# Optimization experiments

Hardware: AMD Instinct MI355X
Metric: run time of the kernel (lower is better)

The kernel has to match this reference:

```python
import jax, jax.numpy as jnp
import numpy as np
import math

D = 768
H = 8
DK = D // H
FF = 1024
EPS = 1e-5


def _layer_norm(x, g, b):
    m = jnp.mean(x, axis=-1, keepdims=True)
    v = jnp.mean((x - m) ** 2, axis=-1, keepdims=True)
    return (x - m) * jax.lax.rsqrt(v + EPS) * g + b


def _mha(x, attention_mask, Wq, bq, Wv, bv, g, b):
    # x: (B,S,D); attention_mask: (B,S,1) bool (True = masked/padding query row)
    B, S, _ = x.shape
    q = (x @ Wq + bq).reshape(B, S, H, DK).transpose(0, 2, 1, 3)  # (B,H,S,dk)
    # NOTE: original code uses the V projection for BOTH k and v (k = self.V(x))
    kv = (x @ Wv + bv).reshape(B, S, H, DK).transpose(0, 2, 1, 3)
    k = kv
    v = kv
    w = jnp.einsum('bhqd,bhkd->bhqk', q, k) / math.sqrt(DK)  # (B,H,S,S)
    pad = attention_mask[:, None, :, :]                      # (B,1,S,1) -> bcast (B,1,S,S)
    causal = jnp.triu(jnp.ones((S, S), dtype=bool), k=1)     # look-ahead mask
    mask = pad | causal
    w = jnp.where(mask, jnp.float32(-1e9), w)
    # NOTE: original uses nn.Softmax(dim=2) -> softmax over the QUERY axis
    score = jax.nn.softmax(w, axis=2)
    o = jnp.einsum('bhqk,bhkd->bhqd', score, v)              # (B,H,S,dk)
    o = o.transpose(0, 2, 1, 3).reshape(B, S, D)
    return _layer_norm(o + x, g, b)


def _ffn(x, W1, b1, W2, b2, g, b):
    h = jax.nn.relu(x @ W1 + b1)
    return _layer_norm(h @ W2 + b2 + x, g, b)


def setup_inputs() -> dict:
    key = jax.random.key(0)
    ks = jax.random.split(key, 16)
    B, S = 8, 1024
    sc = 0.02
    inp = {
        'x': jax.random.normal(ks[0], (B, S, D), dtype=jnp.float32),
        'attention_mask': jax.random.randint(ks[1], (B, S, 1), 0, 2).astype(bool),
    }
    for i, pre in enumerate(['a1', 'a2']):
        inp[pre + '_Wq'] = jax.random.normal(ks[2 + 4 * i], (D, D), dtype=jnp.float32) * sc
        inp[pre + '_bq'] = jnp.zeros((D,), dtype=jnp.float32)
        inp[pre + '_Wv'] = jax.random.normal(ks[3 + 4 * i], (D, D), dtype=jnp.float32) * sc
        inp[pre + '_bv'] = jnp.zeros((D,), dtype=jnp.float32)
        inp[pre + '_g'] = jnp.ones((D,), dtype=jnp.float32)
        inp[pre + '_b'] = jnp.zeros((D,), dtype=jnp.float32)
    inp['f_W1'] = jax.random.normal(ks[10], (D, FF), dtype=jnp.float32) * sc
    inp['f_b1'] = jnp.zeros((FF,), dtype=jnp.float32)
    inp['f_W2'] = jax.random.normal(ks[11], (FF, D), dtype=jnp.float32) * sc
    inp['f_b2'] = jnp.zeros((D,), dtype=jnp.float32)
    inp['f_g'] = jnp.ones((D,), dtype=jnp.float32)
    inp['f_b'] = jnp.zeros((D,), dtype=jnp.float32)
    return inp


def reference(x, attention_mask,
              a1_Wq, a1_bq, a1_Wv, a1_bv, a1_g, a1_b,
              a2_Wq, a2_bq, a2_Wv, a2_bv, a2_g, a2_b,
              f_W1, f_b1, f_W2, f_b2, f_g, f_b):
    x = _mha(x, attention_mask, a1_Wq, a1_bq, a1_Wv, a1_bv, a1_g, a1_b)
    x = _mha(x, attention_mask, a2_Wq, a2_bq, a2_Wv, a2_bv, a2_g, a2_b)
    x = _ffn(x, f_W1, f_b1, f_W2, f_b2, f_g, f_b)
    return x
```

## Files before the change

### kernel.cpp

```cpp
#include <hip/hip_runtime.h>
#include <cstddef>

#define BB 8
#define SS 1024
#define DD 768
#define HH 8
#define DKK 96
#define FFF 1024
#define MM (BB*SS)
#define QVW 1536
#define SM_SCALE 0.10206207261596577f
#define NTILES 16
#define NPAIR  136

typedef unsigned short ushort_t;
typedef short short8 __attribute__((ext_vector_type(8)));
typedef float f32x4 __attribute__((ext_vector_type(4)));
typedef ushort_t us4 __attribute__((ext_vector_type(4)));

__device__ __forceinline__ ushort_t f2b(float f) {
    union { float f; unsigned u; } x; x.f = f;
    unsigned r = x.u + 0x7fffu + ((x.u >> 16) & 1u);
    return (ushort_t)(r >> 16);
}
__device__ __forceinline__ float b2f(ushort_t u) {
    union { unsigned u; float f; } x; x.u = ((unsigned)u) << 16;
    return x.f;
}
__device__ __forceinline__ void gload16(const ushort_t* g, void* lds_base) {
    __builtin_amdgcn_global_load_lds(
        (const __attribute__((address_space(1))) unsigned int*)g,
        (__attribute__((address_space(3))) unsigned int*)lds_base, 16, 0, 0);
}

__global__ __launch_bounds__(256) void castWT(
    const float* __restrict__ W, ushort_t* __restrict__ Wt, int K, int N)
{
    __shared__ float T[32][33];
    const int tx = threadIdx.x & 31, ty = threadIdx.x >> 5;
    const int n0 = blockIdx.x * 32, k0 = blockIdx.y * 32;
    #pragma unroll
    for (int r = 0; r < 4; ++r)
        T[ty + 8*r][tx] = W[(size_t)(k0 + ty + 8*r) * N + n0 + tx];
    __syncthreads();
    #pragma unroll
    for (int r = 0; r < 4; ++r)
        Wt[(size_t)(n0 + ty + 8*r) * K + k0 + tx] = f2b(T[tx][ty + 8*r]);
}

__global__ __launch_bounds__(256) void castWT4(
    const float* __restrict__ Wa, const float* __restrict__ Wb,
    const float* __restrict__ Wc, const float* __restrict__ Wd,
    ushort_t* __restrict__ Ta, ushort_t* __restrict__ Tb,
    ushort_t* __restrict__ Tc, ushort_t* __restrict__ Td)
{
    __shared__ float T[32][33];
    const float* W; ushort_t* Wt;
    switch (blockIdx.z) {
        case 0:  W = Wa; Wt = Ta; break;
        case 1:  W = Wb; Wt = Tb; break;
        case 2:  W = Wc; Wt = Tc; break;
        default: W = Wd; Wt = Td; break;
    }
    const int tx = threadIdx.x & 31, ty = threadIdx.x >> 5;
    const int n0 = blockIdx.x * 32, k0 = blockIdx.y * 32;
    #pragma unroll
    for (int r = 0; r < 4; ++r)
        T[ty + 8*r][tx] = W[(size_t)(k0 + ty + 8*r) * DD + n0 + tx];
    __syncthreads();
    #pragma unroll
    for (int r = 0; r < 4; ++r)
        Wt[(size_t)(n0 + ty + 8*r) * DD + k0 + tx] = f2b(T[tx][ty + 8*r]);
}

__global__ __launch_bounds__(256) void cast_f2b(
    const float* __restrict__ in, ushort_t* __restrict__ out, int n4)
{
    const int i = blockIdx.x * 256 + threadIdx.x;
    if (i >= n4) return;
    const float4 v = ((const float4*)in)[i];
    us4 o; o.x = f2b(v.x); o.y = f2b(v.y); o.z = f2b(v.z); o.w = f2b(v.w);
    ((us4*)out)[i] = o;
}

template<int RELU>
__global__ __launch_bounds__(256) void gemm_bt(
    const ushort_t* __restrict__ A, const ushort_t* __restrict__ Bt,
    const float* __restrict__ bias, const float* __restrict__ bias2, int bN,
    ushort_t* __restrict__ C, int K, int N)
{
    __shared__ ushort_t S[128*136];
    ushort_t* As = S;
    ushort_t* Bs = S + 128*64;
    const int tid  = threadIdx.x;
    const int lane = tid & 63, wave = tid >> 6;
    const int wm = wave >> 1, wn = wave & 1;
    const int n = lane & 15, quad = lane >> 4;
    const int sx = n & 7;
    const int bm = blockIdx.y * 128, bn = blockIdx.x * 128;

    f32x4 acc[4][4];
    #pragma unroll
    for (int i = 0; i < 4; ++i)
        #pragma unroll
        for (int j = 0; j < 4; ++j) acc[i][j] = (f32x4){0.f, 0.f, 0.f, 0.f};

    for (int k0 = 0; k0 < K; k0 += 64) {
        #pragma unroll
        for (int it = 0; it < 4; ++it) {
            const int u   = (it*4 + wave)*64 + lane;
            const int row = u >> 3;
            const int c   = (u & 7) ^ (row & 7);
            gload16(A  + (size_t)(bm + row) * K + k0 + c*8, (char*)As + (it*4 + wave)*1024);
            gload16(Bt + (size_t)(bn + row) * K + k0 + c*8, (char*)Bs + (it*4 + wave)*1024);
        }
        __syncthreads();
        #pragma unroll
        for (int ks = 0; ks < 2; ++ks) {
            short8 af[4], bf[4];
            #pragma unroll
            for (int i = 0; i < 4; ++i)
                af[i] = *(short8*)&As[((wm*64 + i*16 + n)*8 + ((ks*4 + quad) ^ sx))*8];
            #pragma unroll
            for (int j = 0; j < 4; ++j)
                bf[j] = *(short8*)&Bs[((wn*64 + j*16 + n)*8 + ((ks*4 + quad) ^ sx))*8];
            #pragma unroll
            for (int i = 0; i < 4; ++i)
                #pragma unroll
                for (int j = 0; j < 4; ++j)
                    acc[i][j] = __builtin_amdgcn_mfma_f32_16x16x32_bf16(af[i], bf[j], acc[i][j], 0, 0, 0);
        }
        __syncthreads();
    }
    #pragma unroll
    for (int j = 0; j < 4; ++j) {
        const int col = wn*64 + j*16 + n;
        const int gcol = bn + col;
        const float bsv = (gcol < bN) ? bias[gcol] : bias2[gcol - bN];
        #pragma unroll
        for (int i = 0; i < 4; ++i) {
            const int lrow = wm*64 + i*16 + quad*4;
            #pragma unroll
            for (int r = 0; r < 4; ++r) {
                float v = acc[i][j][r] + bsv;
                if (RELU) v = fmaxf(v, 0.f);
                S[(lrow + r)*136 + col] = f2b(v);
            }
        }
    }
    __syncthreads();
    #pragma unroll
    for (int it = 0; it < 8; ++it) {
        const int u = it*256 + tid;
        const int grow = u >> 4, gc = u & 15;
        *(short8*)(C + (size_t)(bm + grow)*N + bn + gc*8) = *(short8*)&S[grow*136 + gc*8];
    }
}

__global__ __launch_bounds__(256) void attn_scores(
    const ushort_t* __restrict__ QV, const int* __restrict__ amask,
    ushort_t* __restrict__ E, float* __restrict__ lpart)
{
    __shared__ ushort_t Qs[64*128];
    __shared__ ushort_t Ks[64*128];
    __shared__ ushort_t Etile[64*72];
    __shared__ float colsum[4][64];
    __shared__ float padf[64];
    const int tid = threadIdx.x, lane = tid & 63, wave = tid >> 6;
    const int n = lane & 15, quad = lane >> 4;
    const int sx = n & 7;
    const int t = blockIdx.x;
    int qt = (int)((-1.f + sqrtf(1.f + 8.f*(float)t)) * 0.5f);
    if ((qt+1)*(qt+2)/2 <= t) ++qt;
    if (qt*(qt+1)/2 > t) --qt;
    const int kt = t - qt*(qt+1)/2;
    const int q0 = qt*64, k0 = kt*64;
    const int h = blockIdx.y, b = blockIdx.z;
    const ushort_t* Qh = QV + (size_t)b*SS*QVW + h*DKK;
    const ushort_t* Kh = QV + (size_t)b*SS*QVW + DD + h*DKK;

    #pragma unroll
    for (int it = 0; it < 4; ++it) {
        const int u = (it*4 + wave)*64 + lane;
        const int row = u >> 4;
        const int c = (u & 15) ^ (row & 7);
        if (c < 12) {
            gload16(Qh + (size_t)(q0 + row)*QVW + c*8, (char*)Qs + (it*4 + wave)*1024);
            gload16(Kh + (size_t)(k0 + row)*QVW + c*8, (char*)Ks + (it*4 + wave)*1024);
        }
    }
    if (tid < 64) padf[tid] = (amask[b*SS + q0 + tid] != 0) ? 1.f : 0.f;
    __syncthreads();

    ushort_t* Et = E + (size_t)(b*HH + h)*NPAIR*4096 + (size_t)(qt*(qt+1)/2 + kt)*4096;

    #pragma unroll
    for (int ns = 0; ns < 4; ++ns) {
        f32x4 sa = (f32x4){0.f, 0.f, 0.f, 0.f};
        #pragma unroll
        for (int ks = 0; ks < 3; ++ks) {
            const short8 aq = *(short8*)&Qs[((wave*16 + n)*16 + ((ks*4 + quad) ^ sx))*8];
            const short8 bk = *(short8*)&Ks[((ns*16   + n)*16 + ((ks*4 + quad) ^ sx))*8];
            sa = __builtin_amdgcn_mfma_f32_16x16x32_bf16(aq, bk, sa, 0, 0, 0);
        }
        const int kl = ns*16 + n;
        const int keyg = k0 + kl;
        float s = 0.f;
        #pragma unroll
        for (int r = 0; r < 4; ++r) {
            const int qrow = wave*16 + quad*4 + r;
            const bool dead = (padf[qrow] != 0.f) || (keyg > q0 + qrow);
            const float e = dead ? 0.f : __expf(sa[r] * SM_SCALE);
            s += e;
            Etile[qrow*72 + kl] = f2b(e);
        }
        s += __shfl_xor(s, 16);
        s += __shfl_xor(s, 32);
        if (quad == 0) colsum[wave][kl] = s;
    }
    __syncthreads();
    #pragma unroll
    for (int it = 0; it < 2; ++it) {
        const int u = it*256 + tid;
        const int grow = u >> 3, gc = u & 7;
        *(short8*)(Et + grow*64 + gc*8) = *(short8*)&Etile[grow*72 + gc*8];
    }
    if (tid < 64) {
        const float s = colsum[0][tid] + colsum[1][tid] + colsum[2][tid] + colsum[3][tid];
        lpart[((size_t)(b*HH + h)*NTILES + qt)*SS + k0 + tid] = s;
    }
}

__global__ __launch_bounds__(256) void transpose_scale(
    const ushort_t* __restrict__ QV, const float* __restrict__ lpart,
    ushort_t* __restrict__ Vt)
{
    __shared__ ushort_t T[64][104];
    __shared__ float rlv[64];
    const int tid = threadIdx.x;
    const int k0 = blockIdx.x * 64, h = blockIdx.y, b = blockIdx.z;
    const ushort_t* src = QV + (size_t)b*SS*QVW + DD + h*DKK;
    for (int s = tid; s < 768; s += 256) {
        const int r = s / 12, c = s % 12;
        *(short8*)&T[r][c*8] = *(const short8*)(src + (size_t)(k0 + r)*QVW + c*8);
    }
    if (tid < 64) {
        const float* lp = lpart + (size_t)(b*HH + h)*NTILES*SS;
        float l = 0.f;
        for (int qt = k0 >> 6; qt < NTILES; ++qt) l += lp[(size_t)qt*SS + k0 + tid];
        rlv[tid] = (l > 0.f) ? (1.f / l) : 0.f;
    }
    __syncthreads();
    ushort_t* dst = Vt + ((size_t)b*HH + h)*DKK*SS;
    for (int s = tid; s < 768; s += 256) {
        const int dk = s >> 3, c = s & 7;
        short8 v;
        #pragma unroll
        for (int i = 0; i < 8; ++i)
            v[i] = (short)f2b(b2f(T[c*8 + i][dk]) * rlv[c*8 + i]);
        *(short8*)(dst + (size_t)dk*SS + k0 + c*8) = v;
    }
}

__global__ __launch_bounds__(256) void attn_pv(
    const ushort_t* __restrict__ E, const ushort_t* __restrict__ Vt,
    ushort_t* __restrict__ O)
{
    __shared__ ushort_t Es[64*64];
    __shared__ ushort_t Vs[96*64];
    const int tid = threadIdx.x, lane = tid & 63, wave = tid >> 6;
    const int n = lane & 15, quad = lane >> 4;
    const int sx = n & 7;
    const int px = blockIdx.x;
    const int h = blockIdx.y, b = blockIdx.z;
    const ushort_t* Eb  = E + (size_t)(b*HH + h)*NPAIR*4096;
    const ushort_t* Vth = Vt + ((size_t)b*HH + h)*DKK*SS;

    #pragma unroll
    for (int half = 0; half < 2; ++half) {
        const int qt = half ? (15 - px) : px;
        const int q0 = qt * 64;
        f32x4 acc[6];
        #pragma unroll
        for (int t = 0; t < 6; ++t) acc[t] = (f32x4){0.f, 0.f, 0.f, 0.f};
        const ushort_t* Eq = Eb + (size_t)(qt*(qt+1)/2)*4096;

        for (int kt = 0; kt <= qt; ++kt) {
            const ushort_t* Et = Eq + (size_t)kt*4096;
            #pragma unroll
            for (int it = 0; it < 2; ++it) {
                const int u = (it*4 + wave)*64 + lane;
                const int row = u >> 3, c = (u & 7) ^ (row & 7);
                gload16(Et + (size_t)row*64 + c*8, (char*)Es + (it*4 + wave)*1024);
            }
            #pragma unroll
            for (int it = 0; it < 3; ++it) {
                const int u = (it*4 + wave)*64 + lane;
                const int row = u >> 3, c = (u & 7) ^ (row & 7);
                gload16(Vth + (size_t)row*SS + kt*64 + c*8, (char*)Vs + (it*4 + wave)*1024);
            }
            __syncthreads();
            #pragma unroll
            for (int kk = 0; kk < 2; ++kk) {
                const short8 ae = *(short8*)&Es[((wave*16 + n)*8 + ((kk*4 + quad) ^ sx))*8];
                #pragma unroll
                for (int nt = 0; nt < 6; ++nt) {
                    const short8 bv = *(short8*)&Vs[((nt*16 + n)*8 + ((kk*4 + quad) ^ sx))*8];
                    acc[nt] = __builtin_amdgcn_mfma_f32_16x16x32_bf16(ae, bv, acc[nt], 0, 0, 0);
                }
            }
            __syncthreads();
        }
        #pragma unroll
        for (int nt = 0; nt < 6; ++nt) {
            #pragma unroll
            for (int r = 0; r < 4; ++r) {
                const int q = q0 + wave*16 + quad*4 + r;
                O[((size_t)b*SS + q)*DD + h*DKK + nt*16 + n] = f2b(acc[nt][r]);
            }
        }
    }
}

__device__ __forceinline__ float block_sum256(float s, float* tmp4)
{
    #pragma unroll
    for (int off = 32; off > 0; off >>= 1) s += __shfl_down(s, off);
    __syncthreads();
    if ((threadIdx.x & 63) == 0) tmp4[threadIdx.x >> 6] = s;
    __syncthreads();
    return tmp4[0] + tmp4[1] + tmp4[2] + tmp4[3];
}

template<int XBF, int RBF, int OUTF32>
__global__ __launch_bounds__(256) void resid_ln(
    const void* __restrict__ X, const void* __restrict__ R,
    const float* __restrict__ g, const float* __restrict__ beta,
    ushort_t* __restrict__ OutB, float* __restrict__ OutF)
{
    __shared__ float tmp4[4];
    const int row = blockIdx.x;
    const int tid = threadIdx.x;
    float v[3], s = 0.f;
    #pragma unroll
    for (int i = 0; i < 3; ++i) {
        const size_t idx = (size_t)row * DD + tid + 256*i;
        const float xv = XBF ? b2f(((const ushort_t*)X)[idx]) : ((const float*)X)[idx];
        const float rv = RBF ? b2f(((const ushort_t*)R)[idx]) : ((const float*)R)[idx];
        v[i] = xv + rv;
        s += v[i];
    }
    const float mu = block_sum256(s, tmp4) * (1.f / DD);
    float qv = 0.f;
    #pragma unroll
    for (int i = 0; i < 3; ++i) { const float d = v[i] - mu; qv += d * d; }
    const float inv = rsqrtf(block_sum256(qv, tmp4) * (1.f / DD) + 1e-5f);
    #pragma unroll
    for (int i = 0; i < 3; ++i) {
        const int c = tid + 256*i;
        const float o = (v[i] - mu) * inv * g[c] + beta[c];
        if (OUTF32) OutF[(size_t)row * DD + c] = o;
        else        OutB[(size_t)row * DD + c] = f2b(o);
    }
}

extern "C" void kernel_launch(void* const* d_in, const int* in_sizes, int n_in,
                              void* d_out, int out_size, void* d_ws, size_t ws_size,
                              hipStream_t stream)
{
    (void)in_sizes; (void)n_in; (void)out_size; (void)ws_size;
    const float* x0    = (const float*)d_in[0];
    const int*   amask = (const int*)d_in[1];
    const float* a1_Wq = (const float*)d_in[2];
    const float* a1_bq = (const float*)d_in[3];
    const float* a1_Wv = (const float*)d_in[4];
    const float* a1_bv = (const float*)d_in[5];
    const float* a1_g  = (const float*)d_in[6];
    const float* a1_b  = (const float*)d_in[7];
    const float* a2_Wq = (const float*)d_in[8];
    const float* a2_bq = (const float*)d_in[9];
    const float* a2_Wv = (const float*)d_in[10];
    const float* a2_bv = (const float*)d_in[11];
    const float* a2_g  = (const float*)d_in[12];
    const float* a2_b  = (const float*)d_in[13];
    const float* f_W1  = (const float*)d_in[14];
    const float* f_b1  = (const float*)d_in[15];
    const float* f_W2  = (const float*)d_in[16];
    const float* f_b2  = (const float*)d_in[17];
    const float* f_g   = (const float*)d_in[18];
    const float* f_b   = (const float*)d_in[19];

    char* ws = (char*)d_ws;
    size_t off = 0;
    auto alloc = [&](size_t bytes) { void* p = ws + off; off += (bytes + 255) & ~(size_t)255; return p; };
    ushort_t* WqvT1 = (ushort_t*)alloc((size_t)QVW*DD*2);
    ushort_t* WqvT2 = (ushort_t*)alloc((size_t)QVW*DD*2);
    ushort_t* W1T   = (ushort_t*)alloc((size_t)DD*FFF*2);
    ushort_t* W2T   = (ushort_t*)alloc((size_t)DD*FFF*2);
    ushort_t* xb0   = (ushort_t*)alloc((size_t)MM*DD*2);
    ushort_t* xb1   = (ushort_t*)alloc((size_t)MM*DD*2);
    ushort_t* xb2   = (ushort_t*)alloc((size_t)MM*DD*2);
    ushort_t* Ob    = (ushort_t*)alloc((size_t)MM*DD*2);
    ushort_t* QVb   = (ushort_t*)alloc((size_t)MM*QVW*2);
    ushort_t* hb    = QVb;
    ushort_t* Vtb   = (ushort_t*)alloc((size_t)MM*DD*2);
    float* lpart = (float*)alloc((size_t)BB*HH*NTILES*SS*4);
    ushort_t* Ebuf = (ushort_t*)alloc((size_t)BB*HH*NPAIR*4096*2);
    float* out = (float*)d_out;

    const dim3 blk(256);
    const dim3 gsc(NPAIR, HH, BB);
    const dim3 gpv(NTILES/2, HH, BB);
    const dim3 gtr(SS/64, HH, BB);
    const dim3 gqv(QVW/128, MM/128);
    const dim3 gf1(FFF/128, MM/128);
    const dim3 gf2(DD/128, MM/128);

    castWT4<<<dim3(DD/32, DD/32, 4), blk, 0, stream>>>(
        a1_Wq, a1_Wv, a2_Wq, a2_Wv,
        WqvT1, WqvT1 + (size_t)DD*DD, WqvT2, WqvT2 + (size_t)DD*DD);
    castWT<<<dim3(FFF/32, DD/32), blk, 0, stream>>>(f_W1, W1T, DD, FFF);
    castWT<<<dim3(DD/32, FFF/32), blk, 0, stream>>>(f_W2, W2T, FFF, DD);
    cast_f2b<<<(MM*DD/4 + 255)/256, blk, 0, stream>>>(x0, xb0, MM*DD/4);

    gemm_bt<0><<<gqv, blk, 0, stream>>>(xb0, WqvT1, a1_bq, a1_bv, DD, QVb, DD, QVW);
    attn_scores<<<gsc, blk, 0, stream>>>(QVb, amask, Ebuf, lpart);
    transpose_scale<<<gtr, blk, 0, stream>>>(QVb, lpart, Vtb);
    attn_pv<<<gpv, blk, 0, stream>>>(Ebuf, Vtb, Ob);
    resid_ln<1,0,0><<<dim3(MM), blk, 0, stream>>>(Ob, x0, a1_g, a1_b, xb1, nullptr);

    gemm_bt<0><<<gqv, blk, 0, stream>>>(xb1, WqvT2, a2_bq, a2_bv, DD, QVb, DD, QVW);
    attn_scores<<<gsc, blk, 0, stream>>>(QVb, amask, Ebuf, lpart);
    transpose_scale<<<gtr, blk, 0, stream>>>(QVb, lpart, Vtb);
    attn_pv<<<gpv, blk, 0, stream>>>(Ebuf, Vtb, Ob);
    resid_ln<1,1,0><<<dim3(MM), blk, 0, stream>>>(Ob, xb1, a2_g, a2_b, xb2, nullptr);

    gemm_bt<1><<<gf1, blk, 0, stream>>>(xb2, W1T, f_b1, f_b1, FFF, hb, DD, FFF);
    gemm_bt<0><<<gf2, blk, 0, stream>>>(hb, W2T, f_b2, f_b2, DD, Ob, FFF, DD);
    resid_ln<1,1,1><<<dim3(MM), blk, 0, stream>>>(Ob, xb2, f_g, f_b, nullptr, out);
}
```

Baseline: 407.1 us.

## Split attention PV over key ranges, load Q/K directly to registers, merge weight casts

attn_pv now splits each query tile's key loop into two halves handled by separate blocks. Each half writes its own partial output buffer, and resid_ln sums the two partials, which doubles the grid to improve occupancy. attn_scores drops its LDS staging of Q/K and reads MFMA fragments straight from global memory with per-lane mask loads. The three weight-cast launches are merged into one. The costs are extra partial-output traffic, idle early-exit blocks in the cast kernel, and uncoalesced fragment loads in attn_scores.

```diff
diff --git a/kernel.cpp b/kernel.cpp
--- a/kernel.cpp
+++ b/kernel.cpp
@@ -33,12 +33,27 @@
         (__attribute__((address_space(3))) unsigned int*)lds_base, 16, 0, 0);
 }
 
-__global__ __launch_bounds__(256) void castWT(
-    const float* __restrict__ W, ushort_t* __restrict__ Wt, int K, int N)
+__global__ __launch_bounds__(256) void castW_all(
+    const float* __restrict__ Wq1, const float* __restrict__ Wv1,
+    const float* __restrict__ Wq2, const float* __restrict__ Wv2,
+    const float* __restrict__ W1,  const float* __restrict__ W2,
+    ushort_t* __restrict__ Tq1, ushort_t* __restrict__ Tv1,
+    ushort_t* __restrict__ Tq2, ushort_t* __restrict__ Tv2,
+    ushort_t* __restrict__ T1,  ushort_t* __restrict__ T2)
 {
     __shared__ float T[32][33];
+    const float* W; ushort_t* Wt; int K, N;
+    switch (blockIdx.z) {
+        case 0:  W = Wq1; Wt = Tq1; K = DD;  N = DD;  break;
+        case 1:  W = Wv1; Wt = Tv1; K = DD;  N = DD;  break;
+        case 2:  W = Wq2; Wt = Tq2; K = DD;  N = DD;  break;
+        case 3:  W = Wv2; Wt = Tv2; K = DD;  N = DD;  break;
+        case 4:  W = W1;  Wt = T1;  K = DD;  N = FFF; break;
+        default: W = W2;  Wt = T2;  K = FFF; N = DD;  break;
+    }
+    const int n0 = blockIdx.x * 32, k0 = blockIdx.y * 32;
+    if (n0 >= N || k0 >= K) return;
     const int tx = threadIdx.x & 31, ty = threadIdx.x >> 5;
-    const int n0 = blockIdx.x * 32, k0 = blockIdx.y * 32;
     #pragma unroll
     for (int r = 0; r < 4; ++r)
         T[ty + 8*r][tx] = W[(size_t)(k0 + ty + 8*r) * N + n0 + tx];
@@ -46,31 +61,6 @@
     #pragma unroll
     for (int r = 0; r < 4; ++r)
         Wt[(size_t)(n0 + ty + 8*r) * K + k0 + tx] = f2b(T[tx][ty + 8*r]);
-}
-
-__global__ __launch_bounds__(256) void castWT4(
-    const float* __restrict__ Wa, const float* __restrict__ Wb,
-    const float* __restrict__ Wc, const float* __restrict__ Wd,
-    ushort_t* __restrict__ Ta, ushort_t* __restrict__ Tb,
-    ushort_t* __restrict__ Tc, ushort_t* __restrict__ Td)
-{
-    __shared__ float T[32][33];
-    const float* W; ushort_t* Wt;
-    switch (blockIdx.z) {
-        case 0:  W = Wa; Wt = Ta; break;
-        case 1:  W = Wb; Wt = Tb; break;
-        case 2:  W = Wc; Wt = Tc; break;
-        default: W = Wd; Wt = Td; break;
-    }
-    const int tx = threadIdx.x & 31, ty = threadIdx.x >> 5;
-    const int n0 = blockIdx.x * 32, k0 = blockIdx.y * 32;
-    #pragma unroll
-    for (int r = 0; r < 4; ++r)
-        T[ty + 8*r][tx] = W[(size_t)(k0 + ty + 8*r) * DD + n0 + tx];
-    __syncthreads();
-    #pragma unroll
-    for (int r = 0; r < 4; ++r)
-        Wt[(size_t)(n0 + ty + 8*r) * DD + k0 + tx] = f2b(T[tx][ty + 8*r]);
 }
 
 __global__ __launch_bounds__(256) void cast_f2b(
@@ -161,14 +151,10 @@
     const ushort_t* __restrict__ QV, const int* __restrict__ amask,
     ushort_t* __restrict__ E, float* __restrict__ lpart)
 {
-    __shared__ ushort_t Qs[64*128];
-    __shared__ ushort_t Ks[64*128];
     __shared__ ushort_t Etile[64*72];
     __shared__ float colsum[4][64];
-    __shared__ float padf[64];
     const int tid = threadIdx.x, lane = tid & 63, wave = tid >> 6;
     const int n = lane & 15, quad = lane >> 4;
-    const int sx = n & 7;
     const int t = blockIdx.x;
     int qt = (int)((-1.f + sqrtf(1.f + 8.f*(float)t)) * 0.5f);
     if ((qt+1)*(qt+2)/2 <= t) ++qt;
@@ -179,37 +165,30 @@
     const ushort_t* Qh = QV + (size_t)b*SS*QVW + h*DKK;
     const ushort_t* Kh = QV + (size_t)b*SS*QVW + DD + h*DKK;
 
-    #pragma unroll
-    for (int it = 0; it < 4; ++it) {
-        const int u = (it*4 + wave)*64 + lane;
-        const int row = u >> 4;
-        const int c = (u & 15) ^ (row & 7);
-        if (c < 12) {
-            gload16(Qh + (size_t)(q0 + row)*QVW + c*8, (char*)Qs + (it*4 + wave)*1024);
-            gload16(Kh + (size_t)(k0 + row)*QVW + c*8, (char*)Ks + (it*4 + wave)*1024);
-        }
-    }
-    if (tid < 64) padf[tid] = (amask[b*SS + q0 + tid] != 0) ? 1.f : 0.f;
-    __syncthreads();
-
-    ushort_t* Et = E + (size_t)(b*HH + h)*NPAIR*4096 + (size_t)(qt*(qt+1)/2 + kt)*4096;
+    const ushort_t* Qrow = Qh + (size_t)(q0 + wave*16 + n)*QVW + quad*8;
+    const short8 qf0 = *(const short8*)(Qrow);
+    const short8 qf1 = *(const short8*)(Qrow + 32);
+    const short8 qf2 = *(const short8*)(Qrow + 64);
+
+    int deadq[4];
+    #pragma unroll
+    for (int r = 0; r < 4; ++r)
+        deadq[r] = amask[b*SS + q0 + wave*16 + quad*4 + r];
 
     #pragma unroll
     for (int ns = 0; ns < 4; ++ns) {
+        const ushort_t* Krow = Kh + (size_t)(k0 + ns*16 + n)*QVW + quad*8;
         f32x4 sa = (f32x4){0.f, 0.f, 0.f, 0.f};
-        #pragma unroll
-        for (int ks = 0; ks < 3; ++ks) {
-            const short8 aq = *(short8*)&Qs[((wave*16 + n)*16 + ((ks*4 + quad) ^ sx))*8];
-            const short8 bk = *(short8*)&Ks[((ns*16   + n)*16 + ((ks*4 + quad) ^ sx))*8];
-            sa = __builtin_amdgcn_mfma_f32_16x16x32_bf16(aq, bk, sa, 0, 0, 0);
-        }
+        sa = __builtin_amdgcn_mfma_f32_16x16x32_bf16(qf0, *(const short8*)(Krow),      sa, 0, 0, 0);
+        sa = __builtin_amdgcn_mfma_f32_16x16x32_bf16(qf1, *(const short8*)(Krow + 32), sa, 0, 0, 0);
+        sa = __builtin_amdgcn_mfma_f32_16x16x32_bf16(qf2, *(const short8*)(Krow + 64), sa, 0, 0, 0);
         const int kl = ns*16 + n;
         const int keyg = k0 + kl;
         float s = 0.f;
         #pragma unroll
         for (int r = 0; r < 4; ++r) {
             const int qrow = wave*16 + quad*4 + r;
-            const bool dead = (padf[qrow] != 0.f) || (keyg > q0 + qrow);
+            const bool dead = (deadq[r] != 0) || (keyg > q0 + qrow);
             const float e = dead ? 0.f : __expf(sa[r] * SM_SCALE);
             s += e;
             Etile[qrow*72 + kl] = f2b(e);
@@ -219,6 +198,8 @@
         if (quad == 0) colsum[wave][kl] = s;
     }
     __syncthreads();
+
+    ushort_t* Et = E + (size_t)(b*HH + h)*NPAIR*4096 + (size_t)(qt*(qt+1)/2 + kt)*4096;
     #pragma unroll
     for (int it = 0; it < 2; ++it) {
         const int u = it*256 + tid;
@@ -264,15 +245,16 @@
 
 __global__ __launch_bounds__(256) void attn_pv(
     const ushort_t* __restrict__ E, const ushort_t* __restrict__ Vt,
-    ushort_t* __restrict__ O)
+    ushort_t* __restrict__ O0, ushort_t* __restrict__ O1)
 {
     __shared__ ushort_t Es[64*64];
     __shared__ ushort_t Vs[96*64];
     const int tid = threadIdx.x, lane = tid & 63, wave = tid >> 6;
     const int n = lane & 15, quad = lane >> 4;
     const int sx = n & 7;
-    const int px = blockIdx.x;
+    const int px = blockIdx.x >> 1, s = blockIdx.x & 1;
     const int h = blockIdx.y, b = blockIdx.z;
+    ushort_t* O = s ? O1 : O0;
     const ushort_t* Eb  = E + (size_t)(b*HH + h)*NPAIR*4096;
     const ushort_t* Vth = Vt + ((size_t)b*HH + h)*DKK*SS;
 
@@ -280,12 +262,15 @@
     for (int half = 0; half < 2; ++half) {
         const int qt = half ? (15 - px) : px;
         const int q0 = qt * 64;
+        const int m   = (qt + 2) >> 1;
+        const int klo = s ? m : 0;
+        const int khi = s ? qt + 1 : m;
         f32x4 acc[6];
         #pragma unroll
         for (int t = 0; t < 6; ++t) acc[t] = (f32x4){0.f, 0.f, 0.f, 0.f};
         const ushort_t* Eq = Eb + (size_t)(qt*(qt+1)/2)*4096;
 
-        for (int kt = 0; kt <= qt; ++kt) {
+        for (int kt = klo; kt < khi; ++kt) {
             const ushort_t* Et = Eq + (size_t)kt*4096;
             #pragma unroll
             for (int it = 0; it < 2; ++it) {
@@ -332,11 +317,12 @@
     return tmp4[0] + tmp4[1] + tmp4[2] + tmp4[3];
 }
 
-template<int XBF, int RBF, int OUTF32>
+template<int XBF, int RBF, int OUTF32, int HAS2>
 __global__ __launch_bounds__(256) void resid_ln(
     const void* __restrict__ X, const void* __restrict__ R,
     const float* __restrict__ g, const float* __restrict__ beta,
-    ushort_t* __restrict__ OutB, float* __restrict__ OutF)
+    ushort_t* __restrict__ OutB, float* __restrict__ OutF,
+    const ushort_t* __restrict__ X2)
 {
     __shared__ float tmp4[4];
     const int row = blockIdx.x;
@@ -347,7 +333,8 @@
         const size_t idx = (size_t)row * DD + tid + 256*i;
         const float xv = XBF ? b2f(((const ushort_t*)X)[idx]) : ((const float*)X)[idx];
         const float rv = RBF ? b2f(((const ushort_t*)R)[idx]) : ((const float*)R)[idx];
-        v[i] = xv + rv;
+        const float x2 = HAS2 ? b2f(X2[idx]) : 0.f;
+        v[i] = xv + x2 + rv;
         s += v[i];
     }
     const float mu = block_sum256(s, tmp4) * (1.f / DD);
@@ -400,7 +387,8 @@
     ushort_t* xb0   = (ushort_t*)alloc((size_t)MM*DD*2);
     ushort_t* xb1   = (ushort_t*)alloc((size_t)MM*DD*2);
     ushort_t* xb2   = (ushort_t*)alloc((size_t)MM*DD*2);
-    ushort_t* Ob    = (ushort_t*)alloc((size_t)MM*DD*2);
+    ushort_t* Op0   = (ushort_t*)alloc((size_t)MM*DD*2);
+    ushort_t* Op1   = (ushort_t*)alloc((size_t)MM*DD*2);
     ushort_t* QVb   = (ushort_t*)alloc((size_t)MM*QVW*2);
     ushort_t* hb    = QVb;
     ushort_t* Vtb   = (ushort_t*)alloc((size_t)MM*DD*2);
@@ -410,32 +398,30 @@
 
     const dim3 blk(256);
     const dim3 gsc(NPAIR, HH, BB);
-    const dim3 gpv(NTILES/2, HH, BB);
+    const dim3 gpv(NTILES, HH, BB);
     const dim3 gtr(SS/64, HH, BB);
     const dim3 gqv(QVW/128, MM/128);
     const dim3 gf1(FFF/128, MM/128);
     const dim3 gf2(DD/128, MM/128);
 
-    castWT4<<<dim3(DD/32, DD/32, 4), blk, 0, stream>>>(
-        a1_Wq, a1_Wv, a2_Wq, a2_Wv,
-        WqvT1, WqvT1 + (size_t)DD*DD, WqvT2, WqvT2 + (size_t)DD*DD);
-    castWT<<<dim3(FFF/32, DD/32), blk, 0, stream>>>(f_W1, W1T, DD, FFF);
-    castWT<<<dim3(DD/32, FFF/32), blk, 0, stream>>>(f_W2, W2T, FFF, DD);
+    castW_all<<<dim3(FFF/32, FFF/32, 6), blk, 0, stream>>>(
+        a1_Wq, a1_Wv, a2_Wq, a2_Wv, f_W1, f_W2,
+        WqvT1, WqvT1 + (size_t)DD*DD, WqvT2, WqvT2 + (size_t)DD*DD, W1T, W2T);
     cast_f2b<<<(MM*DD/4 + 255)/256, blk, 0, stream>>>(x0, xb0, MM*DD/4);
 
     gemm_bt<0><<<gqv, blk, 0, stream>>>(xb0, WqvT1, a1_bq, a1_bv, DD, QVb, DD, QVW);
     attn_scores<<<gsc, blk, 0, stream>>>(QVb, amask, Ebuf, lpart);
     transpose_scale<<<gtr, blk, 0, stream>>>(QVb, lpart, Vtb);
-    attn_pv<<<gpv, blk, 0, stream>>>(Ebuf, Vtb, Ob);
-    resid_ln<1,0,0><<<dim3(MM), blk, 0, stream>>>(Ob, x0, a1_g, a1_b, xb1, nullptr);
+    attn_pv<<<gpv, blk, 0, stream>>>(Ebuf, Vtb, Op0, Op1);
+    resid_ln<1,0,0,1><<<dim3(MM), blk, 0, stream>>>(Op0, x0, a1_g, a1_b, xb1, nullptr, Op1);
 
     gemm_bt<0><<<gqv, blk, 0, stream>>>(xb1, WqvT2, a2_bq, a2_bv, DD, QVb, DD, QVW);
     attn_scores<<<gsc, blk, 0, stream>>>(QVb, amask, Ebuf, lpart);
     transpose_scale<<<gtr, blk, 0, stream>>>(QVb, lpart, Vtb);
-    attn_pv<<<gpv, blk, 0, stream>>>(Ebuf, Vtb, Ob);
-    resid_ln<1,1,0><<<dim3(MM), blk, 0, stream>>>(Ob, xb1, a2_g, a2_b, xb2, nullptr);
+    attn_pv<<<gpv, blk, 0, stream>>>(Ebuf, Vtb, Op0, Op1);
+    resid_ln<1,1,0,1><<<dim3(MM), blk, 0, stream>>>(Op0, xb1, a2_g, a2_b, xb2, nullptr, Op1);
 
     gemm_bt<1><<<gf1, blk, 0, stream>>>(xb2, W1T, f_b1, f_b1, FFF, hb, DD, FFF);
-    gemm_bt<0><<<gf2, blk, 0, stream>>>(hb, W2T, f_b2, f_b2, DD, Ob, FFF, DD);
-    resid_ln<1,1,1><<<dim3(MM), blk, 0, stream>>>(Ob, xb2, f_g, f_b, nullptr, out);
-}
+    gemm_bt<0><<<gf2, blk, 0, stream>>>(hb, W2T, f_b2, f_b2, DD, Op0, FFF, DD);
+    resid_ln<1,1,1,0><<<dim3(MM), blk, 0, stream>>>(Op0, xb2, f_g, f_b, nullptr, out, nullptr);
+}
```

Result: slower. 466.2 us (+14.5%).
